# Performance work log

Hardware: AMD Instinct MI355X
Metric: run time of the kernel (lower is better)

The kernel has to match this reference:

```python
import jax, jax.numpy as jnp
import numpy as np

N = 50000      # nodes
E = 800000     # edges (avg degree 16)
IN = 128       # in_features
OUT = 64       # out_features
NEG_SLOPE = 0.2


def setup_inputs() -> dict:
    key = jax.random.key(0)
    ks = jax.random.split(key, 6)
    x = jax.random.normal(ks[0], (N, IN), dtype=jnp.float32)
    edge_src = jax.random.randint(ks[1], (E,), 0, N, dtype=jnp.int32)  # row i of adj
    edge_dst = jax.random.randint(ks[2], (E,), 0, N, dtype=jnp.int32)  # col j of adj
    stdv = 1.0 / np.sqrt(OUT)
    W = jax.random.uniform(ks[3], (IN, OUT), jnp.float32, -stdv, stdv)
    a = jax.random.uniform(ks[4], (2 * OUT, 1), jnp.float32, -stdv, stdv)
    bias = jax.random.uniform(ks[5], (OUT,), jnp.float32, -stdv, stdv)
    return {"x": x, "W": W, "a": a, "bias": bias,
            "edge_src": edge_src, "edge_dst": edge_dst}


def reference(x, W, a, bias, edge_src, edge_dst):
    # h = input @ weight + bias    [N, OUT]
    h = x @ W + bias
    # Per-node attention halves: Wh1[i] + Wh2[j] == (e = Wh1 + Wh2.T)[i, j]
    Wh1 = h @ a[:OUT, 0]   # [N]
    Wh2 = h @ a[OUT:, 0]   # [N]
    # Edge-centric scores only where adj is nonzero (mirrors e.sparse_mask(adj))
    e = jax.nn.leaky_relu(Wh1[edge_src] + Wh2[edge_dst], NEG_SLOPE)  # [E]
    # Sparse softmax over dim=1 -> segment softmax grouped by source row
    emax = jax.ops.segment_max(e, edge_src, num_segments=N)          # [N]
    ex = jnp.exp(e - emax[edge_src])                                 # [E]
    denom = jax.ops.segment_sum(ex, edge_src, num_segments=N)        # [N]
    alpha = ex / denom[edge_src]                                     # [E]
    # out[i] = sum_j alpha_ij * h[j]  (sparse attention @ h)
    out = jax.ops.segment_sum(alpha[:, None] * h[edge_dst], edge_src,
                              num_segments=N)                        # [N, OUT]
    return out
```

## Files before the change

kernel.cpp:

```cpp
#include <hip/hip_runtime.h>
#include <math.h>


typedef unsigned long long u64;
typedef unsigned int u32;

namespace {
constexpr int NN   = 50000;
constexpr int EE   = 800000;
constexpr int INF_ = 128;
constexpr int OUTF = 64;
constexpr float NEG_SLOPE = 0.2f;
constexpr int MAXDEG = 64;

constexpr int NBUCK   = 196;
constexpr int BCAP    = 4608;
constexpr int S1_CHUNK  = 2048;
constexpr int S1_BLOCKS = (EE + S1_CHUNK - 1) / S1_CHUNK;
constexpr int GEMM_BLOCKS = (NN + 255) / 256;
constexpr int K1_BLOCKS = S1_BLOCKS + GEMM_BLOCKS;
constexpr int S2_BLOCKS = NBUCK * 2;
}

__global__ __launch_bounds__(256)
void gat_fused(const float* __restrict__ x, const float* __restrict__ W,
               const float* __restrict__ av, const float* __restrict__ bias,
               const int* __restrict__ esrc, const int* __restrict__ edst,
               float* __restrict__ h, float* __restrict__ wh1,
               float* __restrict__ wh2, int* __restrict__ bcnt_g,
               u64* __restrict__ bdata)
{
    __shared__ u64 smem[5120];
    const int id  = blockIdx.x;
    const int tid = threadIdx.x;
    const bool is_gemm = (id % 3 == 0) && (id / 3 < GEMM_BLOCKS);

    if (!is_gemm) {
        int ridx = id - id / 3 - ((id % 3) ? 1 : 0);
        if (id % 3 == 0) ridx = GEMM_BLOCKS * 2 + (id / 3 - GEMM_BLOCKS);
        if (id / 3 >= GEMM_BLOCKS && id % 3 == 0) ridx = id - GEMM_BLOCKS;
        else if (id % 3 != 0) ridx = id - id / 3 - 1;
        if (ridx >= S1_BLOCKS) return;

        u64* s_pairs = smem;
        int* s_bcnt  = (int*)((char*)smem + 16384);
        int* s_scan  = s_bcnt + NBUCK;
        int* s_goff  = s_scan + NBUCK;

        for (int i = tid; i < NBUCK; i += 256) s_bcnt[i] = 0;
        __syncthreads();

        const int e0  = ridx * S1_CHUNK;
        const int tot = (EE - e0) < S1_CHUNK ? (EE - e0) : S1_CHUNK;

        int mb[8], mp[8]; u64 mv[8]; int nmine = 0;
#pragma unroll
        for (int k = 0; k < 8; ++k) {
            const int e = e0 + tid + k * 256;
            if (e < e0 + tot) {
                const int s = esrc[e], d = edst[e];
                const int b = s >> 8;
                mb[nmine] = b;
                mp[nmine] = atomicAdd(&s_bcnt[b], 1);
                mv[nmine] = ((u64)(u32)d << 32) | (u32)s;
                ++nmine;
            }
        }
        __syncthreads();
        if (tid < NBUCK) s_scan[tid] = s_bcnt[tid];
        __syncthreads();
        for (int off = 1; off < NBUCK; off <<= 1) {
            int v = 0;
            if (tid < NBUCK && tid >= off) v = s_scan[tid - off];
            __syncthreads();
            if (tid < NBUCK && tid >= off) s_scan[tid] += v;
            __syncthreads();
        }
        if (tid < NBUCK) {
            const int c = s_bcnt[tid];
            s_goff[tid] = c > 0 ? atomicAdd(&bcnt_g[tid], c) : 0;
        }
        __syncthreads();
        for (int k = 0; k < nmine; ++k) {
            const int b = mb[k];
            s_pairs[s_scan[b] - s_bcnt[b] + mp[k]] = mv[k];
        }
        __syncthreads();
        for (int i = tid; i < tot; i += 256) {
            const u64 p = s_pairs[i];
            const int s = (int)(u32)(p & 0xffffffffull);
            const int b = s >> 8;
            const int g = s_goff[b] + (i - (s_scan[b] - s_bcnt[b]));
            if (g < BCAP) bdata[(size_t)b * BCAP + g] = p;
        }
        return;
    }

    float* xT = (float*)smem;
    float* Wc = (float*)((char*)smem + 32768);
    const int ridx  = id / 3;
    const int lane  = tid & 63;
    const int w     = tid >> 6;
    const int node0 = ridx * 256;
    const int ng    = lane & 7;
    const int fg    = lane >> 3;
    const int nbase = w * 64 + ng * 8;
    const int f0    = fg * 8;

    float acc[8][8] = {};

    for (int kc = 0; kc < INF_; kc += 32) {
        __syncthreads();
        {
            const int grow = node0 + tid;
            float4 v[8];
#pragma unroll
            for (int j = 0; j < 8; ++j) v[j] = make_float4(0.f, 0.f, 0.f, 0.f);
            if (grow < NN) {
                const float4* xr = (const float4*)(x + (size_t)grow * INF_ + kc);
#pragma unroll
                for (int j = 0; j < 8; ++j) v[j] = xr[j];
            }
#pragma unroll
            for (int j = 0; j < 8; ++j) {
                xT[(j*4+0)*256 + tid] = v[j].x;
                xT[(j*4+1)*256 + tid] = v[j].y;
                xT[(j*4+2)*256 + tid] = v[j].z;
                xT[(j*4+3)*256 + tid] = v[j].w;
            }
        }
        {
            const float4* wr = (const float4*)(W + (size_t)kc * OUTF);
            float4* wc = (float4*)Wc;
            wc[tid]       = wr[tid];
            wc[tid + 256] = wr[tid + 256];
        }
        __syncthreads();
#pragma unroll 2
        for (int kk = 0; kk < 32; ++kk) {
            const float4 x0 = *(const float4*)&xT[kk * 256 + nbase];
            const float4 x1 = *(const float4*)&xT[kk * 256 + nbase + 4];
            const float4 w0 = *(const float4*)&Wc[kk * 64 + f0];
            const float4 w1 = *(const float4*)&Wc[kk * 64 + f0 + 4];
            const float xa[8] = {x0.x,x0.y,x0.z,x0.w,x1.x,x1.y,x1.z,x1.w};
            const float wa[8] = {w0.x,w0.y,w0.z,w0.w,w1.x,w1.y,w1.z,w1.w};
#pragma unroll
            for (int i = 0; i < 8; ++i)
#pragma unroll
                for (int j = 0; j < 8; ++j) acc[i][j] += xa[i] * wa[j];
        }
    }

    const float4 b0 = ((const float4*)bias)[fg*2];
    const float4 b1 = ((const float4*)bias)[fg*2+1];
    const float4 q0 = ((const float4*)av)[fg*2];
    const float4 q1 = ((const float4*)av)[fg*2+1];
    const float4 r0 = ((const float4*)(av + OUTF))[fg*2];
    const float4 r1 = ((const float4*)(av + OUTF))[fg*2+1];
    const float bb[8]  = {b0.x,b0.y,b0.z,b0.w,b1.x,b1.y,b1.z,b1.w};
    const float a1v[8] = {q0.x,q0.y,q0.z,q0.w,q1.x,q1.y,q1.z,q1.w};
    const float a2v[8] = {r0.x,r0.y,r0.z,r0.w,r1.x,r1.y,r1.z,r1.w};

#pragma unroll
    for (int i = 0; i < 8; ++i) {
        const int node = node0 + nbase + i;
        float p1 = 0.f, p2 = 0.f;
#pragma unroll
        for (int j = 0; j < 8; ++j) {
            acc[i][j] += bb[j];
            p1 += acc[i][j] * a1v[j];
            p2 += acc[i][j] * a2v[j];
        }
        p1 += __shfl_xor(p1, 8); p1 += __shfl_xor(p1, 16); p1 += __shfl_xor(p1, 32);
        p2 += __shfl_xor(p2, 8); p2 += __shfl_xor(p2, 16); p2 += __shfl_xor(p2, 32);
        if (node < NN) {
            float* hp = h + (size_t)node * OUTF + f0;
            *(float4*)hp       = make_float4(acc[i][0], acc[i][1], acc[i][2], acc[i][3]);
            *(float4*)(hp + 4) = make_float4(acc[i][4], acc[i][5], acc[i][6], acc[i][7]);
            if (fg == 0) { wh1[node] = p1; wh2[node] = p2; }
        }
    }
}

__global__ __launch_bounds__(256)
void gat_build(const int* __restrict__ bcnt_g, const u64* __restrict__ bdata,
               int* __restrict__ cnt, int* __restrict__ adj)
{
    __shared__ int l_cnt[128];
    __shared__ int l_adj[128 * 64];
    const int tid    = threadIdx.x;
    const int bid    = blockIdx.x;
    const int bucket = bid >> 1;
    const int node0  = bid << 7;
    if (tid < 128) l_cnt[tid] = 0;
    __syncthreads();

    int n = bcnt_g[bucket];
    n = n > BCAP ? BCAP : n;
    for (int i = tid; i < n; i += 256) {
        const u64 p = bdata[(size_t)bucket * BCAP + i];
        const int s = (int)(u32)(p & 0xffffffffull);
        const int d = (int)(u32)(p >> 32);
        const int ln = s - node0;
        if (ln >= 0 && ln < 128) {
            const int pos = atomicAdd(&l_cnt[ln], 1);
            if (pos < MAXDEG) l_adj[(ln << 6) + pos] = d;
        }
    }
    __syncthreads();

    const int nvalid = (NN - node0) < 128 ? (NN - node0) : 128;
    if (nvalid <= 0) return;
    for (int i = tid; i < nvalid * 64; i += 256)
        adj[((size_t)node0 << 6) + i] = l_adj[i];
    if (tid < nvalid) {
        const int c = l_cnt[tid];
        cnt[node0 + tid] = c > MAXDEG ? MAXDEG : c;
    }
}

__global__ __launch_bounds__(256)
void gat_aggregate(const int* __restrict__ cnt, const int* __restrict__ adj,
                   const float* __restrict__ wh1, const float* __restrict__ wh2,
                   const float* __restrict__ h, float* __restrict__ out)
{
    __shared__ float s_alpha[16 * 65];
    __shared__ int   s_dst[16 * 65];
    const int tid  = threadIdx.x;
    const int wv   = tid >> 6;
    const int lane = tid & 63;
    const int q    = lane >> 4;
    const int f    = lane & 15;
    const int li   = wv * 4 + q;
    const int node = blockIdx.x * 16 + li;

    int deg = cnt[node];
    deg = deg > MAXDEG ? MAXDEG : deg;
    const float w1 = wh1[node];

    float ex[4]; int dl[4]; float el[4];
    float m = -INFINITY;
#pragma unroll
    for (int k = 0; k < 4; ++k) {
        const int slot = f + 16 * k;
        int d = adj[(size_t)node * MAXDEG + slot];
        d = (slot < deg) ? d : 0;
        dl[k] = d;
        float v = w1 + wh2[d];
        v = v > 0.f ? v : NEG_SLOPE * v;
        el[k] = (slot < deg) ? v : -INFINITY;
        m = fmaxf(m, el[k]);
    }
    m = fmaxf(m, __shfl_xor(m, 1)); m = fmaxf(m, __shfl_xor(m, 2));
    m = fmaxf(m, __shfl_xor(m, 4)); m = fmaxf(m, __shfl_xor(m, 8));
    float s = 0.f;
#pragma unroll
    for (int k = 0; k < 4; ++k) {
        ex[k] = (f + 16 * k < deg) ? __expf(el[k] - m) : 0.f;
        s += ex[k];
    }
    s += __shfl_xor(s, 1); s += __shfl_xor(s, 2);
    s += __shfl_xor(s, 4); s += __shfl_xor(s, 8);
    const float inv = (deg > 0) ? 1.f / s : 0.f;

#pragma unroll
    for (int k = 0; k < 4; ++k) {
        s_alpha[li * 65 + f + 16 * k] = ex[k] * inv;
        s_dst  [li * 65 + f + 16 * k] = dl[k];
    }
    __syncthreads();

    float4 acc = make_float4(0.f, 0.f, 0.f, 0.f);
    const int base = li * 65;
    for (int j0 = 0; j0 < deg; j0 += 4) {
        const int i1 = j0 + 1 > 63 ? 63 : j0 + 1;
        const int i2 = j0 + 2 > 63 ? 63 : j0 + 2;
        const int i3 = j0 + 3 > 63 ? 63 : j0 + 3;
        const float a0 = s_alpha[base + j0], a1 = s_alpha[base + i1];
        const float a2 = s_alpha[base + i2], a3 = s_alpha[base + i3];
        const int   d0 = s_dst[base + j0],   d1 = s_dst[base + i1];
        const int   d2 = s_dst[base + i2],   d3 = s_dst[base + i3];
        const float4 v0 = *(const float4*)&h[(size_t)d0 * OUTF + f * 4];
        const float4 v1 = *(const float4*)&h[(size_t)d1 * OUTF + f * 4];
        const float4 v2 = *(const float4*)&h[(size_t)d2 * OUTF + f * 4];
        const float4 v3 = *(const float4*)&h[(size_t)d3 * OUTF + f * 4];
        acc.x += a0*v0.x + a1*v1.x + a2*v2.x + a3*v3.x;
        acc.y += a0*v0.y + a1*v1.y + a2*v2.y + a3*v3.y;
        acc.z += a0*v0.z + a1*v1.z + a2*v2.z + a3*v3.z;
        acc.w += a0*v0.w + a1*v1.w + a2*v2.w + a3*v3.w;
    }
    *(float4*)&out[(size_t)node * OUTF + f * 4] = acc;
}

extern "C" void kernel_launch(void* const* d_in, const int* in_sizes, int n_in,
                              void* d_out, int out_size, void* d_ws, size_t ws_size,
                              hipStream_t stream)
{
    const float* x    = (const float*)d_in[0];
    const float* W    = (const float*)d_in[1];
    const float* av   = (const float*)d_in[2];
    const float* bias = (const float*)d_in[3];
    const int*   esrc = (const int*)d_in[4];
    const int*   edst = (const int*)d_in[5];
    float* out = (float*)d_out;

    float* h      = (float*)d_ws;
    float* wh1    = h + (size_t)NN * OUTF;
    float* wh2    = wh1 + NN;
    int*   cnt    = (int*)(wh2 + NN);
    int*   adj    = cnt + NN;
    int*   bcnt_g = adj + (size_t)NN * MAXDEG;
    u64*   bdata  = (u64*)(bcnt_g + 200);

    hipMemsetAsync(bcnt_g, 0, NBUCK * sizeof(int), stream);
    gat_fused<<<K1_BLOCKS, 256, 0, stream>>>(
        x, W, av, bias, esrc, edst, h, wh1, wh2, bcnt_g, bdata);
    gat_build<<<S2_BLOCKS, 256, 0, stream>>>(bcnt_g, bdata, cnt, adj);
    gat_aggregate<<<NN / 16, 256, 0, stream>>>(cnt, adj, wh1, wh2, h, out);
}
```

Measured before the change: 143.7 us.

## Fuse adjacency build into aggregation and store h as packed bf16

Merges the build and aggregate kernels so each block bins its own 64 nodes from the bucket data into shared memory and computes the softmax and weighted sum directly, removing the global adj/cnt round trip and one launch. The projected features h are now stored as round-to-nearest bf16 pairs, halving the gather traffic in aggregation. In exchange, each bucket is scanned by four blocks instead of two, and the bf16 rounding adds precision error to the output.

```diff
diff --git a/kernel.cpp b/kernel.cpp
--- a/kernel.cpp
+++ b/kernel.cpp
@@ -19,14 +19,21 @@
 constexpr int S1_BLOCKS = (EE + S1_CHUNK - 1) / S1_CHUNK;
 constexpr int GEMM_BLOCKS = (NN + 255) / 256;
 constexpr int K1_BLOCKS = S1_BLOCKS + GEMM_BLOCKS;
-constexpr int S2_BLOCKS = NBUCK * 2;
+constexpr int AGG_BLOCKS = (NN + 63) / 64;
+}
+
+static __device__ __forceinline__ u32 pack2bf(float a, float b) {
+    u32 xa = __builtin_bit_cast(u32, a), xb = __builtin_bit_cast(u32, b);
+    xa = (xa + 0x7fffu + ((xa >> 16) & 1u)) >> 16;
+    xb = (xb + 0x7fffu + ((xb >> 16) & 1u)) >> 16;
+    return xa | (xb << 16);
 }
 
 __global__ __launch_bounds__(256)
 void gat_fused(const float* __restrict__ x, const float* __restrict__ W,
                const float* __restrict__ av, const float* __restrict__ bias,
                const int* __restrict__ esrc, const int* __restrict__ edst,
-               float* __restrict__ h, float* __restrict__ wh1,
+               u32* __restrict__ h16, float* __restrict__ wh1,
                float* __restrict__ wh2, int* __restrict__ bcnt_g,
                u64* __restrict__ bdata)
 {
@@ -174,122 +181,120 @@
         p1 += __shfl_xor(p1, 8); p1 += __shfl_xor(p1, 16); p1 += __shfl_xor(p1, 32);
         p2 += __shfl_xor(p2, 8); p2 += __shfl_xor(p2, 16); p2 += __shfl_xor(p2, 32);
         if (node < NN) {
-            float* hp = h + (size_t)node * OUTF + f0;
-            *(float4*)hp       = make_float4(acc[i][0], acc[i][1], acc[i][2], acc[i][3]);
-            *(float4*)(hp + 4) = make_float4(acc[i][4], acc[i][5], acc[i][6], acc[i][7]);
+            const u32 pk0 = pack2bf(acc[i][0], acc[i][1]);
+            const u32 pk1 = pack2bf(acc[i][2], acc[i][3]);
+            const u32 pk2 = pack2bf(acc[i][4], acc[i][5]);
+            const u32 pk3 = pack2bf(acc[i][6], acc[i][7]);
+            *(uint4*)&h16[(size_t)node * 32 + fg * 4] = make_uint4(pk0, pk1, pk2, pk3);
             if (fg == 0) { wh1[node] = p1; wh2[node] = p2; }
         }
     }
 }
 
 __global__ __launch_bounds__(256)
-void gat_build(const int* __restrict__ bcnt_g, const u64* __restrict__ bdata,
-               int* __restrict__ cnt, int* __restrict__ adj)
+void gat_agg(const int* __restrict__ bcnt_g, const u64* __restrict__ bdata,
+             const float* __restrict__ wh1, const float* __restrict__ wh2,
+             const u32* __restrict__ h16, float* __restrict__ out)
 {
-    __shared__ int l_cnt[128];
-    __shared__ int l_adj[128 * 64];
+    __shared__ int   l_dst[64 * 64];
+    __shared__ float l_alpha[64 * 64];
+    __shared__ int   l_cnt[64];
     const int tid    = threadIdx.x;
     const int bid    = blockIdx.x;
-    const int bucket = bid >> 1;
-    const int node0  = bid << 7;
-    if (tid < 128) l_cnt[tid] = 0;
+    const int node0  = bid << 6;
+    const int bucket = bid >> 2;
+
+    if (tid < 64) l_cnt[tid] = 0;
     __syncthreads();
 
     int n = bcnt_g[bucket];
     n = n > BCAP ? BCAP : n;
     for (int i = tid; i < n; i += 256) {
         const u64 p = bdata[(size_t)bucket * BCAP + i];
-        const int s = (int)(u32)(p & 0xffffffffull);
-        const int d = (int)(u32)(p >> 32);
+        const int s  = (int)(u32)(p & 0xffffffffull);
         const int ln = s - node0;
-        if (ln >= 0 && ln < 128) {
+        if (ln >= 0 && ln < 64) {
             const int pos = atomicAdd(&l_cnt[ln], 1);
-            if (pos < MAXDEG) l_adj[(ln << 6) + pos] = d;
+            if (pos < MAXDEG) l_dst[(ln << 6) + pos] = (int)(u32)(p >> 32);
         }
     }
     __syncthreads();
 
-    const int nvalid = (NN - node0) < 128 ? (NN - node0) : 128;
-    if (nvalid <= 0) return;
-    for (int i = tid; i < nvalid * 64; i += 256)
-        adj[((size_t)node0 << 6) + i] = l_adj[i];
-    if (tid < nvalid) {
-        const int c = l_cnt[tid];
-        cnt[node0 + tid] = c > MAXDEG ? MAXDEG : c;
-    }
-}
-
-__global__ __launch_bounds__(256)
-void gat_aggregate(const int* __restrict__ cnt, const int* __restrict__ adj,
-                   const float* __restrict__ wh1, const float* __restrict__ wh2,
-                   const float* __restrict__ h, float* __restrict__ out)
-{
-    __shared__ float s_alpha[16 * 65];
-    __shared__ int   s_dst[16 * 65];
-    const int tid  = threadIdx.x;
-    const int wv   = tid >> 6;
     const int lane = tid & 63;
-    const int q    = lane >> 4;
+    const int qw   = (tid >> 6) * 4 + (lane >> 4);
     const int f    = lane & 15;
-    const int li   = wv * 4 + q;
-    const int node = blockIdx.x * 16 + li;
-
-    int deg = cnt[node];
-    deg = deg > MAXDEG ? MAXDEG : deg;
-    const float w1 = wh1[node];
-
-    float ex[4]; int dl[4]; float el[4];
-    float m = -INFINITY;
-#pragma unroll
-    for (int k = 0; k < 4; ++k) {
-        const int slot = f + 16 * k;
-        int d = adj[(size_t)node * MAXDEG + slot];
-        d = (slot < deg) ? d : 0;
-        dl[k] = d;
-        float v = w1 + wh2[d];
-        v = v > 0.f ? v : NEG_SLOPE * v;
-        el[k] = (slot < deg) ? v : -INFINITY;
-        m = fmaxf(m, el[k]);
-    }
-    m = fmaxf(m, __shfl_xor(m, 1)); m = fmaxf(m, __shfl_xor(m, 2));
-    m = fmaxf(m, __shfl_xor(m, 4)); m = fmaxf(m, __shfl_xor(m, 8));
-    float s = 0.f;
-#pragma unroll
-    for (int k = 0; k < 4; ++k) {
-        ex[k] = (f + 16 * k < deg) ? __expf(el[k] - m) : 0.f;
-        s += ex[k];
-    }
-    s += __shfl_xor(s, 1); s += __shfl_xor(s, 2);
-    s += __shfl_xor(s, 4); s += __shfl_xor(s, 8);
-    const float inv = (deg > 0) ? 1.f / s : 0.f;
-
-#pragma unroll
-    for (int k = 0; k < 4; ++k) {
-        s_alpha[li * 65 + f + 16 * k] = ex[k] * inv;
-        s_dst  [li * 65 + f + 16 * k] = dl[k];
+
+#pragma unroll
+    for (int nl = 0; nl < 4; ++nl) {
+        const int li   = qw + 16 * nl;
+        const int node = node0 + li;
+        int deg = l_cnt[li];
+        deg = deg > MAXDEG ? MAXDEG : deg;
+        const float w1 = (node < NN) ? wh1[node] : 0.f;
+
+        float el[4]; int dl[4];
+        float m = -INFINITY;
+#pragma unroll
+        for (int k = 0; k < 4; ++k) {
+            const int slot = f + 16 * k;
+            int d = l_dst[(li << 6) + slot];
+            d = (slot < deg) ? d : 0;
+            dl[k] = d;
+            float v = w1 + wh2[d];
+            v = v > 0.f ? v : NEG_SLOPE * v;
+            el[k] = (slot < deg) ? v : -INFINITY;
+            m = fmaxf(m, el[k]);
+        }
+        m = fmaxf(m, __shfl_xor(m, 1)); m = fmaxf(m, __shfl_xor(m, 2));
+        m = fmaxf(m, __shfl_xor(m, 4)); m = fmaxf(m, __shfl_xor(m, 8));
+        float ex[4], s = 0.f;
+#pragma unroll
+        for (int k = 0; k < 4; ++k) {
+            ex[k] = (f + 16 * k < deg) ? __expf(el[k] - m) : 0.f;
+            s += ex[k];
+        }
+        s += __shfl_xor(s, 1); s += __shfl_xor(s, 2);
+        s += __shfl_xor(s, 4); s += __shfl_xor(s, 8);
+        const float inv = (deg > 0) ? 1.f / s : 0.f;
+#pragma unroll
+        for (int k = 0; k < 4; ++k) {
+            l_alpha[(li << 6) + f + 16 * k] = ex[k] * inv;
+            l_dst  [(li << 6) + f + 16 * k] = dl[k];
+        }
     }
     __syncthreads();
 
-    float4 acc = make_float4(0.f, 0.f, 0.f, 0.f);
-    const int base = li * 65;
-    for (int j0 = 0; j0 < deg; j0 += 4) {
-        const int i1 = j0 + 1 > 63 ? 63 : j0 + 1;
-        const int i2 = j0 + 2 > 63 ? 63 : j0 + 2;
-        const int i3 = j0 + 3 > 63 ? 63 : j0 + 3;
-        const float a0 = s_alpha[base + j0], a1 = s_alpha[base + i1];
-        const float a2 = s_alpha[base + i2], a3 = s_alpha[base + i3];
-        const int   d0 = s_dst[base + j0],   d1 = s_dst[base + i1];
-        const int   d2 = s_dst[base + i2],   d3 = s_dst[base + i3];
-        const float4 v0 = *(const float4*)&h[(size_t)d0 * OUTF + f * 4];
-        const float4 v1 = *(const float4*)&h[(size_t)d1 * OUTF + f * 4];
-        const float4 v2 = *(const float4*)&h[(size_t)d2 * OUTF + f * 4];
-        const float4 v3 = *(const float4*)&h[(size_t)d3 * OUTF + f * 4];
-        acc.x += a0*v0.x + a1*v1.x + a2*v2.x + a3*v3.x;
-        acc.y += a0*v0.y + a1*v1.y + a2*v2.y + a3*v3.y;
-        acc.z += a0*v0.z + a1*v1.z + a2*v2.z + a3*v3.z;
-        acc.w += a0*v0.w + a1*v1.w + a2*v2.w + a3*v3.w;
-    }
-    *(float4*)&out[(size_t)node * OUTF + f * 4] = acc;
+#pragma unroll
+    for (int nl = 0; nl < 4; ++nl) {
+        const int li   = qw + 16 * nl;
+        const int node = node0 + li;
+        int deg = l_cnt[li];
+        deg = deg > MAXDEG ? MAXDEG : deg;
+        const int base = li << 6;
+        float4 acc = make_float4(0.f, 0.f, 0.f, 0.f);
+        for (int j0 = 0; j0 < deg; j0 += 4) {
+            const float a0 = l_alpha[base + j0];
+            const float a1 = l_alpha[base + j0 + 1];
+            const float a2 = l_alpha[base + j0 + 2];
+            const float a3 = l_alpha[base + j0 + 3];
+            const int d0 = l_dst[base + j0],     d1 = l_dst[base + j0 + 1];
+            const int d2 = l_dst[base + j0 + 2], d3 = l_dst[base + j0 + 3];
+            const uint2 v0 = *(const uint2*)&h16[(size_t)d0 * 32 + f * 2];
+            const uint2 v1 = *(const uint2*)&h16[(size_t)d1 * 32 + f * 2];
+            const uint2 v2 = *(const uint2*)&h16[(size_t)d2 * 32 + f * 2];
+            const uint2 v3 = *(const uint2*)&h16[(size_t)d3 * 32 + f * 2];
+#define BF_LO(u) __builtin_bit_cast(float, (u) << 16)
+#define BF_HI(u) __builtin_bit_cast(float, (u) & 0xffff0000u)
+            acc.x += a0*BF_LO(v0.x) + a1*BF_LO(v1.x) + a2*BF_LO(v2.x) + a3*BF_LO(v3.x);
+            acc.y += a0*BF_HI(v0.x) + a1*BF_HI(v1.x) + a2*BF_HI(v2.x) + a3*BF_HI(v3.x);
+            acc.z += a0*BF_LO(v0.y) + a1*BF_LO(v1.y) + a2*BF_LO(v2.y) + a3*BF_LO(v3.y);
+            acc.w += a0*BF_HI(v0.y) + a1*BF_HI(v1.y) + a2*BF_HI(v2.y) + a3*BF_HI(v3.y);
+#undef BF_LO
+#undef BF_HI
+        }
+        if (node < NN)
+            *(float4*)&out[(size_t)node * OUTF + f * 4] = acc;
+    }
 }
 
 extern "C" void kernel_launch(void* const* d_in, const int* in_sizes, int n_in,
@@ -304,17 +309,14 @@
     const int*   edst = (const int*)d_in[5];
     float* out = (float*)d_out;
 
-    float* h      = (float*)d_ws;
-    float* wh1    = h + (size_t)NN * OUTF;
+    u32*   h16    = (u32*)d_ws;
+    float* wh1    = (float*)(h16 + (size_t)NN * 32);
     float* wh2    = wh1 + NN;
-    int*   cnt    = (int*)(wh2 + NN);
-    int*   adj    = cnt + NN;
-    int*   bcnt_g = adj + (size_t)NN * MAXDEG;
+    int*   bcnt_g = (int*)(wh2 + NN);
     u64*   bdata  = (u64*)(bcnt_g + 200);
 
     hipMemsetAsync(bcnt_g, 0, NBUCK * sizeof(int), stream);
     gat_fused<<<K1_BLOCKS, 256, 0, stream>>>(
-        x, W, av, bias, esrc, edst, h, wh1, wh2, bcnt_g, bdata);
-    gat_build<<<S2_BLOCKS, 256, 0, stream>>>(bcnt_g, bdata, cnt, adj);
-    gat_aggregate<<<NN / 16, 256, 0, stream>>>(cnt, adj, wh1, wh2, h, out);
-}
+        x, W, av, bias, esrc, edst, h16, wh1, wh2, bcnt_g, bdata);
+    gat_agg<<<AGG_BLOCKS, 256, 0, stream>>>(bcnt_g, bdata, wh1, wh2, h16, out);
+}
```

Result: faster. 134.4 us (-6.4%).
